# Optimization experiments

Hardware: AMD Instinct MI355X
Metric: run time of the kernel (lower is better)

The kernel has to match this reference:

```python
import jax, jax.numpy as jnp
import numpy as np

N_SUBJECTS = 16
N_LABELS = 8
DENS_TEMP = 0.1  # args.ProtoSim_dens_temp


def setup_inputs() -> dict:
    key = jax.random.key(0)
    k1, k2, k3 = jax.random.split(key, 3)
    B, V, D = 131072, 2, 128
    X_data = jax.random.normal(k1, (B, V, D), dtype=jnp.float32)
    subject = jax.random.randint(k2, (B,), 0, N_SUBJECTS, dtype=jnp.int64) if jax.config.read('jax_enable_x64') else jax.random.randint(k2, (B,), 0, N_SUBJECTS)
    labels = jax.random.randint(k3, (B,), 0, N_LABELS)
    return {"X_data": X_data, "subject": subject, "labels": labels}


def reference(X_data, subject, labels):
    B, V, D = X_data.shape
    G = N_SUBJECTS * N_LABELS
    # torch.cat(torch.unbind(X_data, dim=1), dim=0): view-major ordering -> [V*B, D]
    cf = jnp.transpose(X_data, (1, 0, 2)).reshape(V * B, D)
    # subject/labels duplicated once (module assumes 2 views)
    seg = jnp.tile(subject * N_LABELS + labels, V)  # group id per row, [V*B]
    counts = jax.ops.segment_sum(jnp.ones((V * B,), jnp.float32), seg, num_segments=G)
    centroid = jax.ops.segment_sum(cf, seg, num_segments=G) / counts[:, None]  # [G, D]
    # per-point euclidean distance to own group centroid (torch.cdist to 1-row centroid)
    dist = jnp.linalg.norm(cf - centroid[seg], axis=1)  # [V*B]
    # density: mean(sqrt(dist)) / log(n + 10) for groups with n > 1, else 0 then dmax
    dens = (jax.ops.segment_sum(jnp.sqrt(dist), seg, num_segments=G) / counts) / jnp.log(counts + 10.0)
    dens = jnp.where(counts > 1, dens, 0.0)
    dens = jnp.where(counts > 1, dens, dens.max())
    lo = jnp.percentile(dens, 10.0)
    hi = jnp.percentile(dens, 90.0)
    dens = jnp.clip(dens, lo, hi)
    dens = DENS_TEMP * dens / dens.mean()
    cen_of_cen = centroid.mean(axis=0)  # [D]
    sim = jnp.exp((centroid @ cen_of_cen) / dens)  # [G]
    sim = sim - sim.max()
    return -sim.mean()
```

## Files before the change

kernel.cpp:

```cpp
#include <hip/hip_runtime.h>
#include <cstdint>
#include <cstddef>

#define BPTS    131072
#define D_DIM   128
#define G_GR    128
#define NL      8
#define GD      (G_GR * D_DIM)
#define NBLK    512
#define TPB     512
#define PPB     (BPTS / NBLK)
#define PPW     (PPB / 8)
#define DRB     16

__device__ __forceinline__ float dpp_add(float d, const int ctrl) {
    int s;
    switch (ctrl) {
    case 0x111: s = __builtin_amdgcn_update_dpp(0, __float_as_int(d), 0x111, 0xf, 0xf, true); break;
    case 0x112: s = __builtin_amdgcn_update_dpp(0, __float_as_int(d), 0x112, 0xf, 0xf, true); break;
    case 0x114: s = __builtin_amdgcn_update_dpp(0, __float_as_int(d), 0x114, 0xf, 0xf, true); break;
    case 0x118: s = __builtin_amdgcn_update_dpp(0, __float_as_int(d), 0x118, 0xf, 0xf, true); break;
    case 0x142: s = __builtin_amdgcn_update_dpp(0, __float_as_int(d), 0x142, 0xf, 0xf, true); break;
    default:    s = __builtin_amdgcn_update_dpp(0, __float_as_int(d), 0x143, 0xf, 0xf, true); break;
    }
    return d + __int_as_float(s);
}

__device__ __forceinline__ float sum64(float d) {
    d = dpp_add(d, 0x111);
    d = dpp_add(d, 0x112);
    d = dpp_add(d, 0x114);
    d = dpp_add(d, 0x118);
    d = dpp_add(d, 0x142);
    d = dpp_add(d, 0x143);
    return d;
}

__global__ __launch_bounds__(TPB) void k_centroid(const float* __restrict__ Xf,
                                                  const int* __restrict__ sub,
                                                  const int* __restrict__ lab,
                                                  float* __restrict__ cpart,
                                                  int* __restrict__ hpart) {
    __shared__ float bins[GD];
    __shared__ int   hist[G_GR];
    int t = threadIdx.x, blk = blockIdx.x;
    int lane = t & 63, w = t >> 6;

    for (int i = t; i < GD; i += TPB) bins[i] = 0.f;
    if (t < G_GR) hist[t] = 0;

    int base = blk * PPB + w * PPW;
    int pl = base + (lane & 31);
    int gv = sub[pl] * NL + lab[pl];
    __syncthreads();

    if (lane < 32) atomicAdd(&hist[gv], 1);

    for (int it = 0; it < PPW / 8; ++it) {
        int p0 = base + it * 8;
        float x0[8], x1[8], x2[8], x3[8];
#pragma unroll
        for (int u = 0; u < 8; ++u) {
            const float* r = Xf + (size_t)(p0 + u) * 256;
            x0[u] = r[lane];
            x1[u] = r[64  + lane];
            x2[u] = r[128 + lane];
            x3[u] = r[192 + lane];
        }
#pragma unroll
        for (int u = 0; u < 8; ++u) {
            int g = __builtin_amdgcn_readlane(gv, it * 8 + u);
            float vlo = x0[u] + x2[u];
            float vhi = x1[u] + x3[u];
            atomicAdd(&bins[g * D_DIM + lane],      vlo);
            atomicAdd(&bins[g * D_DIM + 64 + lane], vhi);
        }
    }
    __syncthreads();
    for (int i = t; i < GD; i += TPB)
        cpart[(size_t)blk * GD + i] = bins[i];
    if (t < G_GR) hpart[blk * G_GR + t] = hist[t];
}

__global__ __launch_bounds__(512) void k_reduce(const float* __restrict__ cpart,
                                                const int* __restrict__ hpart,
                                                float* __restrict__ centroid,
                                                float* __restrict__ countsf) {
    __shared__ float red[8][64];
    __shared__ int   hred[64];
    __shared__ float cf2s;
    int g = blockIdx.x >> 1, h = blockIdx.x & 1;
    int t = threadIdx.x;
    int dl = t & 63, bs = t >> 6;
    int d = h * 64 + dl;

    float acc = 0.f;
    for (int b = bs; b < NBLK; b += 8)
        acc += cpart[(size_t)b * GD + g * D_DIM + d];
    red[bs][dl] = acc;

    if (t < 64) {
        int hacc = 0;
        for (int b = t; b < NBLK; b += 64) hacc += hpart[b * G_GR + g];
        hred[t] = hacc;
    }
    __syncthreads();
    if (t == 0) {
        int n = 0;
        for (int i = 0; i < 64; ++i) n += hred[i];
        cf2s = 2.f * (float)n;
        if (h == 0) countsf[g] = cf2s;
    }
    __syncthreads();
    if (t < 64) {
        float v = 0.f;
#pragma unroll
        for (int r = 0; r < 8; ++r) v += red[r][t];
        float cf2 = cf2s;
        centroid[g * D_DIM + h * 64 + t] = (cf2 > 0.f) ? v / cf2 : 0.f;
    }
}

__global__ __launch_bounds__(TPB) void k_distn(const float* __restrict__ Xf,
                                               const int* __restrict__ sub,
                                               const int* __restrict__ lab,
                                               const float* __restrict__ centroid,
                                               float* __restrict__ dpart) {
    __shared__ float cen[GD];
    __shared__ float dbin[G_GR];
    int t = threadIdx.x, blk = blockIdx.x;
    int lane = t & 63, w = t >> 6;

    for (int i = t; i < GD; i += TPB) cen[i] = centroid[i];
    if (t < G_GR) dbin[t] = 0.f;

    int base = blk * PPB + w * PPW;
    int pl = base + (lane & 31);
    int gv = sub[pl] * NL + lab[pl];
    __syncthreads();

    float dacc = 0.f;
    for (int it = 0; it < PPW / 8; ++it) {
        int p0 = base + it * 8;
        float x0[8], x1[8], x2[8], x3[8];
#pragma unroll
        for (int u = 0; u < 8; ++u) {
            const float* r = Xf + (size_t)(p0 + u) * 256;
            x0[u] = r[lane];
            x1[u] = r[64  + lane];
            x2[u] = r[128 + lane];
            x3[u] = r[192 + lane];
        }
#pragma unroll
        for (int u = 0; u < 8; ++u) {
            int g = __builtin_amdgcn_readlane(gv, it * 8 + u);
            float c_lo = cen[g * D_DIM + lane];
            float c_hi = cen[g * D_DIM + 64 + lane];
            float e0 = x0[u] - c_lo, e1 = x1[u] - c_hi;
            float e2 = x2[u] - c_lo, e3 = x3[u] - c_hi;
            float d0 = sum64(e0 * e0 + e1 * e1);
            float d1 = sum64(e2 * e2 + e3 * e3);
            float s0 = __int_as_float(__builtin_amdgcn_readlane(__float_as_int(d0), 63));
            float s1 = __int_as_float(__builtin_amdgcn_readlane(__float_as_int(d1), 63));
            float st = sqrtf(sqrtf(s0)) + sqrtf(sqrtf(s1));
            if (lane == it * 8 + u) dacc += st;
        }
    }
    if (lane < 32) atomicAdd(&dbin[gv], dacc);
    __syncthreads();
    if (t < G_GR) dpart[blk * G_GR + t] = dbin[t];
}

__global__ __launch_bounds__(256) void k_dred(const float* __restrict__ dpart,
                                              float* __restrict__ dmid) {
    __shared__ float red[2][G_GR];
    int t = threadIdx.x, blk = blockIdx.x;
    int d = t & 127, h = t >> 7;
    int b0 = blk * (NBLK / DRB);
    float acc = 0.f;
    for (int b = b0 + h; b < b0 + NBLK / DRB; b += 2)
        acc += dpart[b * G_GR + d];
    red[h][d] = acc;
    __syncthreads();
    if (t < G_GR) dmid[blk * G_GR + t] = red[0][t] + red[1][t];
}

__global__ __launch_bounds__(128) void k_final(const float* __restrict__ dmid,
                                               const float* __restrict__ countsf,
                                               const float* __restrict__ centroid,
                                               float* __restrict__ out) {
    __shared__ float srt[G_GR];
    __shared__ float red[G_GR];
    __shared__ float coc[D_DIM];
    int t = threadIdx.x;

    float ds = 0.f;
    for (int b = 0; b < DRB; ++b) ds += dmid[b * G_GR + t];
    float cnt  = countsf[t];
    float dens = (cnt > 1.f) ? (ds / cnt) / logf(cnt + 10.f) : 0.f;

    red[t] = dens;
    __syncthreads();
    for (int s = 64; s > 0; s >>= 1) {
        if (t < s) red[t] = fmaxf(red[t], red[t + s]);
        __syncthreads();
    }
    float dmax = red[0];
    __syncthreads();
    if (!(cnt > 1.f)) dens = dmax;

    srt[t] = dens;
    __syncthreads();
    for (int k = 2; k <= G_GR; k <<= 1) {
        for (int j = k >> 1; j > 0; j >>= 1) {
            int ixj = t ^ j;
            if (ixj > t) {
                float a = srt[t], b = srt[ixj];
                bool up = ((t & k) == 0);
                if ((a > b) == up) { srt[t] = b; srt[ixj] = a; }
            }
            __syncthreads();
        }
    }
    double p10 = 0.10 * 127.0, p90 = 0.90 * 127.0;
    int   i10 = (int)p10,           i90 = (int)p90;
    float f10 = (float)(p10 - i10), f90 = (float)(p90 - i90);
    float lo = srt[i10] + f10 * (srt[i10 + 1] - srt[i10]);
    float hi = srt[i90] + f90 * (srt[i90 + 1] - srt[i90]);
    dens = fminf(fmaxf(dens, lo), hi);

    red[t] = dens;
    __syncthreads();
    for (int s = 64; s > 0; s >>= 1) {
        if (t < s) red[t] += red[t + s];
        __syncthreads();
    }
    float dmean = red[0] / 128.f;
    __syncthreads();
    dens = 0.1f * dens / dmean;

    float cs = 0.f;
    for (int g = 0; g < G_GR; ++g) cs += centroid[g * D_DIM + t];
    coc[t] = cs / 128.f;
    __syncthreads();

    float dot = 0.f;
    for (int d = 0; d < D_DIM; ++d) dot += centroid[t * D_DIM + d] * coc[d];
    float sim = expf(dot / dens);

    red[t] = sim;
    __syncthreads();
    for (int s = 64; s > 0; s >>= 1) {
        if (t < s) red[t] = fmaxf(red[t], red[t + s]);
        __syncthreads();
    }
    float smax = red[0];
    __syncthreads();
    red[t] = sim - smax;
    __syncthreads();
    for (int s = 64; s > 0; s >>= 1) {
        if (t < s) red[t] += red[t + s];
        __syncthreads();
    }
    if (t == 0) out[0] = -(red[0] / 128.f);
}

extern "C" void kernel_launch(void* const* d_in, const int* in_sizes, int n_in,
                              void* d_out, int out_size, void* d_ws, size_t ws_size,
                              hipStream_t stream) {
    const float*  Xf      = (const float*)d_in[0];
    const int*    subject = (const int*)d_in[1];
    const int*    labels  = (const int*)d_in[2];
    float*        out     = (float*)d_out;
    char*         ws      = (char*)d_ws;

    size_t o = 0;
    float* cpart    = (float*)(ws + o); o += (size_t)NBLK * GD * 4;
    int*   hpart    = (int*)(ws + o);   o += (size_t)NBLK * G_GR * 4;
    float* centroid = (float*)(ws + o); o += (size_t)GD * 4;
    float* countsf  = (float*)(ws + o); o += 512;
    float* dpart    = (float*)(ws + o); o += (size_t)NBLK * G_GR * 4;
    float* dmid     = (float*)(ws + o); o += (size_t)DRB * G_GR * 4;

    k_centroid<<<NBLK, TPB, 0, stream>>>(Xf, subject, labels, cpart, hpart);
    k_reduce  <<<G_GR * 2, 512, 0, stream>>>(cpart, hpart, centroid, countsf);
    k_distn   <<<NBLK, TPB, 0, stream>>>(Xf, subject, labels, centroid, dpart);
    k_dred    <<<DRB, 256, 0, stream>>>(dpart, dmid);
    k_final   <<<1, 128, 0, stream>>>(dmid, countsf, centroid, out);
}
```

Measured before the change: 293.6 us.

## Bucket points by group per block, replacing LDS atomics with per-wave group sums

Each block now counting-sorts its 256 points by group id using a shared histogram, a prefix scan and a cursor, giving per-group point lists. Each wave then owns 8 groups and accumulates their rows in registers, writing partial centroids directly. This removes the 64 KB LDS bins and the per-element shared atomics, and drops centroid staging into LDS in the distance kernel. Block size doubles to 1024. In exchange, loads become gathers with short dependent loops per group (about 2 points per group per block), which can hurt memory-level parallelism, and each kernel now pays several barriers for the scan.

Measured after the change: 271.4 us. 7.6% less time.

```diff
diff --git a/kernel.cpp b/kernel.cpp
--- a/kernel.cpp
+++ b/kernel.cpp
@@ -8,9 +8,9 @@
 #define NL      8
 #define GD      (G_GR * D_DIM)
 #define NBLK    512
-#define TPB     512
+#define TPB     1024
 #define PPB     (BPTS / NBLK)
-#define PPW     (PPB / 8)
+#define GPW     (G_GR / (TPB / 64))
 #define DRB     16
 
 __device__ __forceinline__ float dpp_add(float d, const int ctrl) {
@@ -36,50 +36,82 @@
     return d;
 }
 
+__device__ __forceinline__ void build_lists(const int* __restrict__ sub,
+                                            const int* __restrict__ lab,
+                                            int pbase, int t,
+                                            int* glist, int* goff,
+                                            int* hist, int* cursor, int* scan) {
+    if (t < G_GR) hist[t] = 0;
+    __syncthreads();
+    int myg = -1;
+    if (t < PPB) {
+        myg = sub[pbase + t] * NL + lab[pbase + t];
+        atomicAdd(&hist[myg], 1);
+    }
+    __syncthreads();
+    if (t < G_GR) scan[t] = hist[t];
+    __syncthreads();
+    for (int s = 1; s < G_GR; s <<= 1) {
+        int v = 0;
+        if (t < G_GR) { v = scan[t]; if (t >= s) v += scan[t - s]; }
+        __syncthreads();
+        if (t < G_GR) scan[t] = v;
+        __syncthreads();
+    }
+    if (t < G_GR) { goff[t] = scan[t] - hist[t]; cursor[t] = scan[t] - hist[t]; }
+    __syncthreads();
+    if (t < PPB) {
+        int pos = atomicAdd(&cursor[myg], 1);
+        glist[pos] = t;
+    }
+    __syncthreads();
+}
+
 __global__ __launch_bounds__(TPB) void k_centroid(const float* __restrict__ Xf,
                                                   const int* __restrict__ sub,
                                                   const int* __restrict__ lab,
                                                   float* __restrict__ cpart,
                                                   int* __restrict__ hpart) {
-    __shared__ float bins[GD];
-    __shared__ int   hist[G_GR];
+    __shared__ int glist[PPB];
+    __shared__ int goff[G_GR];
+    __shared__ int hist[G_GR];
+    __shared__ int cursor[G_GR];
+    __shared__ int scan[G_GR];
     int t = threadIdx.x, blk = blockIdx.x;
     int lane = t & 63, w = t >> 6;
-
-    for (int i = t; i < GD; i += TPB) bins[i] = 0.f;
-    if (t < G_GR) hist[t] = 0;
-
-    int base = blk * PPB + w * PPW;
-    int pl = base + (lane & 31);
-    int gv = sub[pl] * NL + lab[pl];
-    __syncthreads();
-
-    if (lane < 32) atomicAdd(&hist[gv], 1);
-
-    for (int it = 0; it < PPW / 8; ++it) {
-        int p0 = base + it * 8;
-        float x0[8], x1[8], x2[8], x3[8];
-#pragma unroll
-        for (int u = 0; u < 8; ++u) {
-            const float* r = Xf + (size_t)(p0 + u) * 256;
-            x0[u] = r[lane];
-            x1[u] = r[64  + lane];
-            x2[u] = r[128 + lane];
-            x3[u] = r[192 + lane];
+    int pbase = blk * PPB;
+
+    build_lists(sub, lab, pbase, t, glist, goff, hist, cursor, scan);
+    if (t < G_GR) hpart[blk * G_GR + t] = hist[t];
+
+    for (int gi = 0; gi < GPW; ++gi) {
+        int g = w * GPW + gi;
+        int s = goff[g], n = hist[g];
+        float ax = 0.f, ay = 0.f;
+        int k = 0;
+        for (; k + 2 <= n; k += 2) {
+            int p0 = pbase + glist[s + k];
+            int p1 = pbase + glist[s + k + 1];
+            const float* r0 = Xf + (size_t)p0 * 256;
+            const float* r1 = Xf + (size_t)p1 * 256;
+            float2 a0 = *(const float2*)(r0 + 2 * lane);
+            float2 b0 = *(const float2*)(r0 + 128 + 2 * lane);
+            float2 a1 = *(const float2*)(r1 + 2 * lane);
+            float2 b1 = *(const float2*)(r1 + 128 + 2 * lane);
+            ax += (a0.x + b0.x) + (a1.x + b1.x);
+            ay += (a0.y + b0.y) + (a1.y + b1.y);
         }
-#pragma unroll
-        for (int u = 0; u < 8; ++u) {
-            int g = __builtin_amdgcn_readlane(gv, it * 8 + u);
-            float vlo = x0[u] + x2[u];
-            float vhi = x1[u] + x3[u];
-            atomicAdd(&bins[g * D_DIM + lane],      vlo);
-            atomicAdd(&bins[g * D_DIM + 64 + lane], vhi);
+        if (k < n) {
+            int p = pbase + glist[s + k];
+            const float* r = Xf + (size_t)p * 256;
+            float2 a = *(const float2*)(r + 2 * lane);
+            float2 b = *(const float2*)(r + 128 + 2 * lane);
+            ax += a.x + b.x;
+            ay += a.y + b.y;
         }
-    }
-    __syncthreads();
-    for (int i = t; i < GD; i += TPB)
-        cpart[(size_t)blk * GD + i] = bins[i];
-    if (t < G_GR) hpart[blk * G_GR + t] = hist[t];
+        float2 o; o.x = ax; o.y = ay;
+        *(float2*)(cpart + (size_t)blk * GD + (size_t)g * D_DIM + 2 * lane) = o;
+    }
 }
 
 __global__ __launch_bounds__(512) void k_reduce(const float* __restrict__ cpart,
@@ -126,49 +158,35 @@
                                                const int* __restrict__ lab,
                                                const float* __restrict__ centroid,
                                                float* __restrict__ dpart) {
-    __shared__ float cen[GD];
-    __shared__ float dbin[G_GR];
+    __shared__ int glist[PPB];
+    __shared__ int goff[G_GR];
+    __shared__ int hist[G_GR];
+    __shared__ int cursor[G_GR];
+    __shared__ int scan[G_GR];
     int t = threadIdx.x, blk = blockIdx.x;
     int lane = t & 63, w = t >> 6;
-
-    for (int i = t; i < GD; i += TPB) cen[i] = centroid[i];
-    if (t < G_GR) dbin[t] = 0.f;
-
-    int base = blk * PPB + w * PPW;
-    int pl = base + (lane & 31);
-    int gv = sub[pl] * NL + lab[pl];
-    __syncthreads();
-
-    float dacc = 0.f;
-    for (int it = 0; it < PPW / 8; ++it) {
-        int p0 = base + it * 8;
-        float x0[8], x1[8], x2[8], x3[8];
-#pragma unroll
-        for (int u = 0; u < 8; ++u) {
-            const float* r = Xf + (size_t)(p0 + u) * 256;
-            x0[u] = r[lane];
-            x1[u] = r[64  + lane];
-            x2[u] = r[128 + lane];
-            x3[u] = r[192 + lane];
+    int pbase = blk * PPB;
+
+    build_lists(sub, lab, pbase, t, glist, goff, hist, cursor, scan);
+
+    for (int gi = 0; gi < GPW; ++gi) {
+        int g = w * GPW + gi;
+        int s = goff[g], n = hist[g];
+        float2 c = *(const float2*)(centroid + (size_t)g * D_DIM + 2 * lane);
+        float sacc = 0.f;
+        for (int k = 0; k < n; ++k) {
+            int p = pbase + glist[s + k];
+            const float* r = Xf + (size_t)p * 256;
+            float2 a = *(const float2*)(r + 2 * lane);
+            float2 b = *(const float2*)(r + 128 + 2 * lane);
+            float e0 = a.x - c.x, e1 = a.y - c.y;
+            float f0 = b.x - c.x, f1 = b.y - c.y;
+            float d0 = sum64(e0 * e0 + e1 * e1);
+            float d1 = sum64(f0 * f0 + f1 * f1);
+            sacc += sqrtf(sqrtf(d0)) + sqrtf(sqrtf(d1));
         }
-#pragma unroll
-        for (int u = 0; u < 8; ++u) {
-            int g = __builtin_amdgcn_readlane(gv, it * 8 + u);
-            float c_lo = cen[g * D_DIM + lane];
-            float c_hi = cen[g * D_DIM + 64 + lane];
-            float e0 = x0[u] - c_lo, e1 = x1[u] - c_hi;
-            float e2 = x2[u] - c_lo, e3 = x3[u] - c_hi;
-            float d0 = sum64(e0 * e0 + e1 * e1);
-            float d1 = sum64(e2 * e2 + e3 * e3);
-            float s0 = __int_as_float(__builtin_amdgcn_readlane(__float_as_int(d0), 63));
-            float s1 = __int_as_float(__builtin_amdgcn_readlane(__float_as_int(d1), 63));
-            float st = sqrtf(sqrtf(s0)) + sqrtf(sqrtf(s1));
-            if (lane == it * 8 + u) dacc += st;
-        }
-    }
-    if (lane < 32) atomicAdd(&dbin[gv], dacc);
-    __syncthreads();
-    if (t < G_GR) dpart[blk * G_GR + t] = dbin[t];
+        if (lane == 63) dpart[blk * G_GR + g] = sacc;
+    }
 }
 
 __global__ __launch_bounds__(256) void k_dred(const float* __restrict__ dpart,
```
